# Kernel tuning notes

Measured on AMD Instinct MI355X. Metric: run time of the kernel, lower is better.

The kernel has to match this reference:

```python
import jax, jax.numpy as jnp
import numpy as np

N_HEAD, D_MODEL, D_K, D_V, POS_DIM = 8, 512, 64, 64, 2
TEMPERATURE = 8.0
LN_EPS = 1e-6


def setup_inputs() -> dict:
    key = jax.random.key(0)
    ks = jax.random.split(key, 16)
    B, S = 4, 1024
    s = 0.02
    return {
        "q": jax.random.normal(ks[0], (B, S, D_MODEL), jnp.float32),
        "k": jax.random.normal(ks[1], (B, S, D_MODEL), jnp.float32),
        "v": jax.random.normal(ks[2], (B, S, D_MODEL), jnp.float32),
        "pos_mat": jax.random.normal(ks[3], (S, S, POS_DIM), jnp.float32),
        "w_qs": jax.random.normal(ks[4], (N_HEAD * D_K, D_MODEL), jnp.float32) * s,
        "w_ks": jax.random.normal(ks[5], (N_HEAD * D_K, D_MODEL), jnp.float32) * s,
        "w_vs": jax.random.normal(ks[6], (N_HEAD * D_V, D_MODEL), jnp.float32) * s,
        "w_fc": jax.random.normal(ks[7], (D_MODEL, N_HEAD * D_V), jnp.float32) * s,
        "rp_w1": jax.random.normal(ks[8], (D_K, POS_DIM), jnp.float32) * s,
        "rp_b1": jnp.zeros((D_K,), jnp.float32),
        "rp_w2": jax.random.normal(ks[9], (D_K, D_K), jnp.float32) * s,
        "rp_b2": jnp.zeros((D_K,), jnp.float32),
        "ln_g": jnp.ones((D_MODEL,), jnp.float32),
        "ln_b": jnp.zeros((D_MODEL,), jnp.float32),
    }


def reference(q, k, v, pos_mat, w_qs, w_ks, w_vs, w_fc, rp_w1, rp_b1, rp_w2, rp_b2, ln_g, ln_b):
    B, S, _ = q.shape
    residual = q
    # projections -> (b, h, s, d)
    Q = (q @ w_qs.T).reshape(B, S, N_HEAD, D_K).transpose(0, 2, 1, 3)
    K = (k @ w_ks.T).reshape(B, S, N_HEAD, D_K).transpose(0, 2, 1, 3)
    V = (v @ w_vs.T).reshape(B, S, N_HEAD, D_V).transpose(0, 2, 1, 3)
    # relative position embedding: (s, s, d_k)
    a_k = jnp.tanh  # placeholder name avoided; compute MLP (no nonlinearity in original)
    a_k = (pos_mat @ rp_w1.T + rp_b1) @ rp_w2.T + rp_b2
    # sum over d_k of elementwise q*k*a_k, without materializing (b,h,q,k,d)
    attn = jnp.einsum("bhqd,bhkd,qkd->bhqk", Q, K, a_k) / TEMPERATURE
    attn = jax.nn.softmax(attn, axis=-1)  # dropout disabled (eval)
    out = jnp.einsum("bhqk,bhkd->bhqd", attn, V)  # (b,h,s,d_v)
    out = out.transpose(0, 2, 1, 3).reshape(B, S, N_HEAD * D_V)
    out = out @ w_fc.T + residual
    # layer norm
    mu = out.mean(-1, keepdims=True)
    var = out.var(-1, keepdims=True)
    out = (out - mu) / jnp.sqrt(var + LN_EPS) * ln_g + ln_b
    return (out, attn)
```

## Files before the change

kernel.cpp:

```cpp
#include <hip/hip_runtime.h>
#include <math.h>

#define NB   4
#define SEQ  1024
#define DMOD 512
#define NHD  8
#define DK   64

typedef unsigned short ushort_t;
typedef __attribute__((ext_vector_type(8))) short bf16x8;
typedef __attribute__((ext_vector_type(4))) float f32x4;

#define XQ_OFF   1024
#define XK_OFF   (XQ_OFF + 4194304)
#define XV_OFF   (XK_OFF + 4194304)
#define WQ_OFF   (XV_OFF + 4194304)
#define WK_OFF   (WQ_OFF + 524288)
#define WV_OFF   (WK_OFF + 524288)
#define WF_OFF   (WV_OFF + 524288)
#define QBF_OFF  (WF_OFF + 524288)
#define KBF_OFF  (QBF_OFF + 4194304)
#define VT_OFF   (KBF_OFF + 12582912)
#define POSBF_OFF XQ_OFF
#define O2_OFF   XQ_OFF
#define OBF_OFF  XV_OFF

__device__ inline ushort_t f2bf(float x) {
    unsigned u = __builtin_bit_cast(unsigned, x);
    unsigned r = (u + 0x7FFFu + ((u >> 16) & 1u)) >> 16;
    return (ushort_t)r;
}
__device__ inline unsigned pk2(float a, float b) {
    return (unsigned)f2bf(a) | ((unsigned)f2bf(b) << 16);
}

__global__ __launch_bounds__(256)
void setup_kernel(const float* __restrict__ pos,
                  const float* __restrict__ w_qs, const float* __restrict__ w_ks,
                  const float* __restrict__ w_vs, const float* __restrict__ w_fc,
                  const float* __restrict__ rp_w1, const float* __restrict__ rp_b1,
                  const float* __restrict__ rp_w2, const float* __restrict__ rp_b2,
                  unsigned* __restrict__ posbf,
                  ushort_t* __restrict__ WQ, ushort_t* __restrict__ WK,
                  ushort_t* __restrict__ WV, ushort_t* __restrict__ WF,
                  float* __restrict__ ws)
{
    const int bid = blockIdx.x;
    const int tid = threadIdx.x;
    if (bid < 1024) {
        int t = bid * 256 + tid;
        float4 a = *(const float4*)&pos[t * 8];
        float4 b = *(const float4*)&pos[t * 8 + 4];
        uint4 o = {pk2(a.x, a.y), pk2(a.z, a.w), pk2(b.x, b.y), pk2(b.z, b.w)};
        *(uint4*)&posbf[t * 4] = o;
    } else if (bid < 2048) {
        int which = (bid - 1024) >> 8;
        int t = ((bid - 1024) & 255) * 256 + tid;
        const float* s = (which == 0) ? w_qs : (which == 1) ? w_ks
                       : (which == 2) ? w_vs : w_fc;
        ushort_t* d = (which == 0) ? WQ : (which == 1) ? WK
                    : (which == 2) ? WV : WF;
        float4 v = *(const float4*)&s[t * 4];
        uint2 o = {pk2(v.x, v.y), pk2(v.z, v.w)};
        *(uint2*)&d[t * 4] = o;
    } else {
        __shared__ float red[4][64][3];
        int d = tid & 63, p = tid >> 6;
        float w0 = 0.f, w1 = 0.f, cc = 0.f;
        #pragma unroll
        for (int jj = 0; jj < 16; jj++) {
            int j = p * 16 + jj;
            float r2 = rp_w2[d * 64 + j];
            w0 += r2 * rp_w1[j * 2 + 0];
            w1 += r2 * rp_w1[j * 2 + 1];
            cc += r2 * rp_b1[j];
        }
        red[p][d][0] = w0; red[p][d][1] = w1; red[p][d][2] = cc;
        __syncthreads();
        if (p == 0) {
            w0 = red[0][d][0] + red[1][d][0] + red[2][d][0] + red[3][d][0];
            w1 = red[0][d][1] + red[1][d][1] + red[2][d][1] + red[3][d][1];
            cc = red[0][d][2] + red[1][d][2] + red[2][d][2] + red[3][d][2];
            ws[d] = cc + rp_b2[d];
            ws[64 + 2 * d + 0] = w0;
            ws[64 + 2 * d + 1] = w1;
        }
    }
}

#define GP 72

__global__ __launch_bounds__(256)
void mfma_gemm_qkv(const float* __restrict__ xq, const float* __restrict__ xk,
                   const float* __restrict__ xv,
                   const ushort_t* __restrict__ wq, const ushort_t* __restrict__ wk,
                   const ushort_t* __restrict__ wv,
                   ushort_t* __restrict__ Qbf, ushort_t* __restrict__ Kbf,
                   ushort_t* __restrict__ Vt, const float* __restrict__ wc)
{
    __shared__ ushort_t Sb[12800];
    ushort_t* Xs = Sb;
    ushort_t* Ws = Sb + 64 * GP;
    const int bz = blockIdx.z;
    const float* X = (bz == 0) ? xq : (bz == 1) ? xk : xv;
    const ushort_t* Wt = (bz == 0) ? wq : (bz == 1) ? wk : wv;
    const int n0 = blockIdx.y * 64;
    const int o0 = blockIdx.x * 64;
    const int tid = threadIdx.x;
    const int wave = tid >> 6, lane = tid & 63;
    const int m16 = lane & 15, g = lane >> 4;

    f32x4 acc[4] = {};
    for (int m0 = 0; m0 < 512; m0 += 64) {
        #pragma unroll
        for (int it = 0; it < 2; it++) {
            int idx = tid + it * 256;
            int row = idx >> 3, c8 = (idx & 7) * 8;
            float4 a = *(const float4*)&X[(n0 + row) * 512 + m0 + c8];
            float4 b = *(const float4*)&X[(n0 + row) * 512 + m0 + c8 + 4];
            uint4 o = {pk2(a.x, a.y), pk2(a.z, a.w), pk2(b.x, b.y), pk2(b.z, b.w)};
            *(uint4*)&Xs[row * GP + c8] = o;
            *(uint4*)&Ws[row * GP + c8] = *(const uint4*)&Wt[(o0 + row) * 512 + m0 + c8];
        }
        __syncthreads();
        #pragma unroll
        for (int kc = 0; kc < 2; kc++) {
            bf16x8 a = *(const bf16x8*)&Xs[(wave * 16 + m16) * GP + kc * 32 + g * 8];
            #pragma unroll
            for (int to = 0; to < 4; to++) {
                bf16x8 b = *(const bf16x8*)&Ws[(to * 16 + m16) * GP + kc * 32 + g * 8];
                acc[to] = __builtin_amdgcn_mfma_f32_16x16x32_bf16(a, b, acc[to], 0, 0, 0);
            }
        }
        __syncthreads();
    }

    const int b = n0 >> 10, s0 = n0 & 1023, h = o0 >> 6;
    const int bh = b * NHD + h;
    const int srow = wave * 16 + g * 4;

    if (bz == 0) {
        #pragma unroll
        for (int to = 0; to < 4; to++)
            #pragma unroll
            for (int r = 0; r < 4; r++)
                Sb[(srow + r) * GP + to * 16 + m16] = f2bf(acc[to][r]);
        __syncthreads();
        #pragma unroll
        for (int it = 0; it < 2; it++) {
            int cid = tid + it * 256;
            int row = cid >> 3, c8 = (cid & 7) * 8;
            *(uint4*)&Qbf[((bh << 10) + s0 + row) * 64 + c8] =
                *(const uint4*)&Sb[row * GP + c8];
        }
    } else if (bz == 1) {
        #pragma unroll
        for (int to = 0; to < 4; to++) {
            int d = to * 16 + m16;
            float c0 = wc[d], c1 = wc[64 + 2 * d], c2 = wc[64 + 2 * d + 1];
            #pragma unroll
            for (int r = 0; r < 4; r++) {
                float a = acc[to][r];
                int rb = (srow + r) * 200 + d;
                Sb[rb]       = f2bf(a * c0);
                Sb[rb + 64]  = f2bf(a * c1);
                Sb[rb + 128] = f2bf(a * c2);
            }
        }
        __syncthreads();
        #pragma unroll
        for (int it = 0; it < 6; it++) {
            int cid = tid + it * 256;
            int row = cid / 24, c = cid % 24;
            *(uint4*)&Kbf[((bh << 10) + s0 + row) * 192 + c * 8] =
                *(const uint4*)&Sb[row * 200 + c * 8];
        }
    } else {
        #pragma unroll
        for (int to = 0; to < 4; to++)
            #pragma unroll
            for (int r = 0; r < 4; r++)
                Sb[(to * 16 + m16) * GP + srow + r] = f2bf(acc[to][r]);
        __syncthreads();
        #pragma unroll
        for (int it = 0; it < 2; it++) {
            int cid = tid + it * 256;
            int row = cid >> 3, c8 = (cid & 7) * 8;
            *(uint4*)&Vt[(bh * 64 + row) * 1024 + s0 + c8] =
                *(const uint4*)&Sb[row * GP + c8];
        }
    }
}

__global__ __launch_bounds__(256)
void mfma_gemm_fc(const ushort_t* __restrict__ X, const ushort_t* __restrict__ Wt,
                  float* __restrict__ ofp, const float* __restrict__ resid)
{
    __shared__ ushort_t Xs[64 * GP];
    __shared__ ushort_t Ws[64 * GP];
    const int n0 = blockIdx.y * 64;
    const int o0 = blockIdx.x * 64;
    const int tid = threadIdx.x;
    const int wave = tid >> 6, lane = tid & 63;
    const int m16 = lane & 15, g = lane >> 4;

    f32x4 acc[4] = {};
    for (int m0 = 0; m0 < 512; m0 += 64) {
        #pragma unroll
        for (int it = 0; it < 2; it++) {
            int idx = tid + it * 256;
            int row = idx >> 3, c8 = (idx & 7) * 8;
            *(uint4*)&Xs[row * GP + c8] = *(const uint4*)&X[(n0 + row) * 512 + m0 + c8];
            *(uint4*)&Ws[row * GP + c8] = *(const uint4*)&Wt[(o0 + row) * 512 + m0 + c8];
        }
        __syncthreads();
        #pragma unroll
        for (int kc = 0; kc < 2; kc++) {
            bf16x8 a = *(const bf16x8*)&Xs[(wave * 16 + m16) * GP + kc * 32 + g * 8];
            #pragma unroll
            for (int to = 0; to < 4; to++) {
                bf16x8 b = *(const bf16x8*)&Ws[(to * 16 + m16) * GP + kc * 32 + g * 8];
                acc[to] = __builtin_amdgcn_mfma_f32_16x16x32_bf16(a, b, acc[to], 0, 0, 0);
            }
        }
        __syncthreads();
    }
    #pragma unroll
    for (int to = 0; to < 4; to++) {
        int o = o0 + to * 16 + m16;
        #pragma unroll
        for (int r = 0; r < 4; r++) {
            int n = n0 + wave * 16 + g * 4 + r;
            ofp[n * 512 + o] = acc[to][r] + resid[n * 512 + o];
        }
    }
}

#define QPITCH 72
#define KPLANE (64 * QPITCH + 8)
#define POSP 68
__global__ __launch_bounds__(256)
void fused_attn(const ushort_t* __restrict__ Qbf, const ushort_t* __restrict__ Kbf,
                const unsigned* __restrict__ posu, const ushort_t* __restrict__ Vt,
                float* __restrict__ attn, ushort_t* __restrict__ Obf)
{
    __shared__ ushort_t Ks[3 * KPLANE];
    __shared__ ushort_t Vs[64 * QPITCH];
    __shared__ ushort_t Ps[64 * QPITCH];
    __shared__ unsigned PosS[64 * POSP];
    const int bh = blockIdx.x;
    const int q0 = blockIdx.y * 64;
    const int tid = threadIdx.x;
    const int wave = tid >> 6, lane = tid & 63;
    const int m16 = lane & 15, g = lane >> 4;

    const ushort_t* qrow = &Qbf[((bh << 10) + q0 + wave * 16 + m16) * 64];
    bf16x8 qf0 = *(const bf16x8*)&qrow[g * 8];
    bf16x8 qf1 = *(const bf16x8*)&qrow[32 + g * 8];

    float l[4] = {0.f, 0.f, 0.f, 0.f};

    for (int k0 = 0; k0 < 1024; k0 += 64) {
        #pragma unroll
        for (int it = 0; it < 6; it++) {
            int idx = tid + it * 256;
            int row = idx / 24, c = idx % 24;
            int j = c >> 3, d8 = (c & 7) * 8;
            *(uint4*)&Ks[j * KPLANE + row * QPITCH + d8] =
                *(const uint4*)&Kbf[((bh << 10) + k0 + row) * 192 + c * 8];
        }
        #pragma unroll
        for (int it = 0; it < 4; it++) {
            int idx = tid + it * 256;
            int row = idx >> 4, c4 = (idx & 15) * 4;
            *(uint4*)&PosS[row * POSP + c4] =
                *(const uint4*)&posu[(q0 + row) * 1024 + k0 + c4];
        }
        __syncthreads();

        f32x4 sc[4][3] = {};
        #pragma unroll
        for (int kc = 0; kc < 2; kc++) {
            bf16x8 af = kc ? qf1 : qf0;
            #pragma unroll
            for (int tk = 0; tk < 4; tk++)
                #pragma unroll
                for (int j = 0; j < 3; j++) {
                    bf16x8 bfv = *(const bf16x8*)&Ks[j * KPLANE + (tk * 16 + m16) * QPITCH + kc * 32 + g * 8];
                    sc[tk][j] = __builtin_amdgcn_mfma_f32_16x16x32_bf16(af, bfv, sc[tk][j], 0, 0, 0);
                }
        }

        #pragma unroll
        for (int r = 0; r < 4; r++) {
            #pragma unroll
            for (int tk = 0; tk < 4; tk++) {
                unsigned pu = PosS[(wave * 16 + g * 4 + r) * POSP + tk * 16 + m16];
                float p0 = __builtin_bit_cast(float, pu << 16);
                float p1 = __builtin_bit_cast(float, pu & 0xFFFF0000u);
                float s = (sc[tk][0][r] + p0 * sc[tk][1][r] + p1 * sc[tk][2][r]) * 0.125f;
                l[r] += __expf(s);
            }
        }
        __syncthreads();
    }
    float inv_l[4];
    #pragma unroll
    for (int r = 0; r < 4; r++) {
        float s = l[r];
        #pragma unroll
        for (int msk = 1; msk < 16; msk <<= 1) s += __shfl_xor(s, msk, 64);
        inv_l[r] = 1.0f / s;
    }

    f32x4 ao[4] = {};
    for (int k0 = 0; k0 < 1024; k0 += 64) {
        #pragma unroll
        for (int it = 0; it < 6; it++) {
            int idx = tid + it * 256;
            int row = idx / 24, c = idx % 24;
            int j = c >> 3, d8 = (c & 7) * 8;
            *(uint4*)&Ks[j * KPLANE + row * QPITCH + d8] =
                *(const uint4*)&Kbf[((bh << 10) + k0 + row) * 192 + c * 8];
        }
        #pragma unroll
        for (int it = 0; it < 2; it++) {
            int idx = tid + it * 256;
            int row = idx >> 3, c8 = (idx & 7) * 8;
            *(uint4*)&Vs[row * QPITCH + c8] = *(const uint4*)&Vt[(bh * 64 + row) * 1024 + k0 + c8];
        }
        #pragma unroll
        for (int it = 0; it < 4; it++) {
            int idx = tid + it * 256;
            int row = idx >> 4, c4 = (idx & 15) * 4;
            *(uint4*)&PosS[row * POSP + c4] =
                *(const uint4*)&posu[(q0 + row) * 1024 + k0 + c4];
        }
        __syncthreads();

        f32x4 sc[4][3] = {};
        #pragma unroll
        for (int kc = 0; kc < 2; kc++) {
            bf16x8 af = kc ? qf1 : qf0;
            #pragma unroll
            for (int tk = 0; tk < 4; tk++)
                #pragma unroll
                for (int j = 0; j < 3; j++) {
                    bf16x8 bfv = *(const bf16x8*)&Ks[j * KPLANE + (tk * 16 + m16) * QPITCH + kc * 32 + g * 8];
                    sc[tk][j] = __builtin_amdgcn_mfma_f32_16x16x32_bf16(af, bfv, sc[tk][j], 0, 0, 0);
                }
        }

        #pragma unroll
        for (int r = 0; r < 4; r++) {
            int q = q0 + wave * 16 + g * 4 + r;
            #pragma unroll
            for (int tk = 0; tk < 4; tk++) {
                unsigned pu = PosS[(wave * 16 + g * 4 + r) * POSP + tk * 16 + m16];
                float p0 = __builtin_bit_cast(float, pu << 16);
                float p1 = __builtin_bit_cast(float, pu & 0xFFFF0000u);
                float s = (sc[tk][0][r] + p0 * sc[tk][1][r] + p1 * sc[tk][2][r]) * 0.125f;
                float p = __expf(s) * inv_l[r];
                attn[((bh << 10) + q) * 1024 + k0 + tk * 16 + m16] = p;
                Ps[(wave * 16 + g * 4 + r) * QPITCH + tk * 16 + m16] = f2bf(p);
            }
        }
        __syncthreads();

        #pragma unroll
        for (int kc = 0; kc < 2; kc++) {
            bf16x8 a = *(const bf16x8*)&Ps[(wave * 16 + m16) * QPITCH + kc * 32 + g * 8];
            #pragma unroll
            for (int td = 0; td < 4; td++) {
                bf16x8 b = *(const bf16x8*)&Vs[(td * 16 + m16) * QPITCH + kc * 32 + g * 8];
                ao[td] = __builtin_amdgcn_mfma_f32_16x16x32_bf16(a, b, ao[td], 0, 0, 0);
            }
        }
        __syncthreads();
    }

    const int b = bh >> 3, h = bh & 7;
    #pragma unroll
    for (int td = 0; td < 4; td++) {
        int d = td * 16 + m16;
        #pragma unroll
        for (int r = 0; r < 4; r++) {
            int q = q0 + wave * 16 + g * 4 + r;
            Obf[((b << 10) + q) * 512 + h * 64 + d] = f2bf(ao[td][r]);
        }
    }
}

__global__ __launch_bounds__(256)
void ln_kernel(const float* __restrict__ X, const float* __restrict__ g,
               const float* __restrict__ bta, float* __restrict__ out)
{
    const int row = blockIdx.x;
    const int tid = threadIdx.x;
    float2 x = *(const float2*)&X[row * 512 + tid * 2];
    float s  = x.x + x.y;
    float s2 = x.x * x.x + x.y * x.y;
    for (int off = 32; off; off >>= 1) {
        s  += __shfl_down(s, off, 64);
        s2 += __shfl_down(s2, off, 64);
    }
    __shared__ float rs[4], rs2[4];
    __shared__ float mu_s, rstd_s;
    int wave = tid >> 6, lane = tid & 63;
    if (lane == 0) { rs[wave] = s; rs2[wave] = s2; }
    __syncthreads();
    if (tid == 0) {
        float S1 = rs[0] + rs[1] + rs[2] + rs[3];
        float S2 = rs2[0] + rs2[1] + rs2[2] + rs2[3];
        float mu = S1 * (1.0f / 512.0f);
        float var = S2 * (1.0f / 512.0f) - mu * mu;
        mu_s = mu;
        rstd_s = rsqrtf(var + 1e-6f);
    }
    __syncthreads();
    float mu = mu_s, rstd = rstd_s;
    float2 gv = *(const float2*)&g[tid * 2];
    float2 bv = *(const float2*)&bta[tid * 2];
    float2 o;
    o.x = (x.x - mu) * rstd * gv.x + bv.x;
    o.y = (x.y - mu) * rstd * gv.y + bv.y;
    *(float2*)&out[row * 512 + tid * 2] = o;
}

extern "C" void kernel_launch(void* const* d_in, const int* in_sizes, int n_in,
                              void* d_out, int out_size, void* d_ws, size_t ws_size,
                              hipStream_t stream)
{
    const float* q       = (const float*)d_in[0];
    const float* k       = (const float*)d_in[1];
    const float* v       = (const float*)d_in[2];
    const float* pos_mat = (const float*)d_in[3];
    const float* w_qs    = (const float*)d_in[4];
    const float* w_ks    = (const float*)d_in[5];
    const float* w_vs    = (const float*)d_in[6];
    const float* w_fc    = (const float*)d_in[7];
    const float* rp_w1   = (const float*)d_in[8];
    const float* rp_b1   = (const float*)d_in[9];
    const float* rp_w2   = (const float*)d_in[10];
    const float* rp_b2   = (const float*)d_in[11];
    const float* ln_g    = (const float*)d_in[12];
    const float* ln_b    = (const float*)d_in[13];

    char* wsb = (char*)d_ws;
    float*    wc  = (float*)d_ws;
    ushort_t* WQ  = (ushort_t*)(wsb + WQ_OFF);
    ushort_t* WK  = (ushort_t*)(wsb + WK_OFF);
    ushort_t* WV  = (ushort_t*)(wsb + WV_OFF);
    ushort_t* WF  = (ushort_t*)(wsb + WF_OFF);
    ushort_t* Qbf = (ushort_t*)(wsb + QBF_OFF);
    ushort_t* Kbf = (ushort_t*)(wsb + KBF_OFF);
    ushort_t* Vt  = (ushort_t*)(wsb + VT_OFF);
    float*    O2  = (float*)(wsb + O2_OFF);
    ushort_t* Obf = (ushort_t*)(wsb + OBF_OFF);
    unsigned* Pbf = (unsigned*)(wsb + POSBF_OFF);

    float* out  = (float*)d_out;
    float* attn = out + 2097152;

    setup_kernel<<<dim3(2049), 256, 0, stream>>>(pos_mat, w_qs, w_ks, w_vs, w_fc,
                                                 rp_w1, rp_b1, rp_w2, rp_b2,
                                                 Pbf, WQ, WK, WV, WF, wc);

    mfma_gemm_qkv<<<dim3(8, 64, 3), 256, 0, stream>>>(q, k, v, WQ, WK, WV,
                                                      Qbf, Kbf, Vt, wc);

    fused_attn<<<dim3(32, 16), 256, 0, stream>>>(Qbf, Kbf, Pbf, Vt, attn, Obf);

    mfma_gemm_fc<<<dim3(8, 64), 256, 0, stream>>>(Obf, WF, O2, q);
    ln_kernel<<<dim3(4096), 256, 0, stream>>>(O2, ln_g, ln_b, out);
}
```

Before: 305.4 us.

## Double-buffer LDS tiles in QKV and FC GEMMs with register prefetch

Both projection GEMMs now prefetch the next K-slice from global memory into registers while the MFMAs consume the current tile. The staged data is then written to a second LDS buffer, which leaves one barrier per iteration instead of two. The grid axes are also swapped so consecutive blocks walk along rows rather than output columns, which changes L2 reuse of the activation and weight tiles. The cost is a larger LDS footprint (36KB) and more live registers, which may reduce occupancy.

```diff
diff --git a/kernel.cpp b/kernel.cpp
--- a/kernel.cpp
+++ b/kernel.cpp
@@ -98,31 +98,46 @@
                    ushort_t* __restrict__ Qbf, ushort_t* __restrict__ Kbf,
                    ushort_t* __restrict__ Vt, const float* __restrict__ wc)
 {
-    __shared__ ushort_t Sb[12800];
-    ushort_t* Xs = Sb;
-    ushort_t* Ws = Sb + 64 * GP;
+    __shared__ ushort_t SH[18432];
     const int bz = blockIdx.z;
     const float* X = (bz == 0) ? xq : (bz == 1) ? xk : xv;
     const ushort_t* Wt = (bz == 0) ? wq : (bz == 1) ? wk : wv;
-    const int n0 = blockIdx.y * 64;
-    const int o0 = blockIdx.x * 64;
+    const int n0 = blockIdx.x * 64;
+    const int o0 = blockIdx.y * 64;
     const int tid = threadIdx.x;
     const int wave = tid >> 6, lane = tid & 63;
     const int m16 = lane & 15, g = lane >> 4;
+    const int sr = tid >> 3, sc8 = (tid & 7) * 8;
+
+    float4 xa0, xb0, xa1, xb1;
+    uint4  wr0, wr1;
+
+#define LOADT(m0_) { \
+    xa0 = *(const float4*)&X[(n0 + sr) * 512 + (m0_) + sc8]; \
+    xb0 = *(const float4*)&X[(n0 + sr) * 512 + (m0_) + sc8 + 4]; \
+    xa1 = *(const float4*)&X[(n0 + sr + 32) * 512 + (m0_) + sc8]; \
+    xb1 = *(const float4*)&X[(n0 + sr + 32) * 512 + (m0_) + sc8 + 4]; \
+    wr0 = *(const uint4*)&Wt[(o0 + sr) * 512 + (m0_) + sc8]; \
+    wr1 = *(const uint4*)&Wt[(o0 + sr + 32) * 512 + (m0_) + sc8]; }
+#define STORET(b_) { \
+    ushort_t* Xs_ = SH + (b_) * 4608; \
+    ushort_t* Ws_ = SH + 9216 + (b_) * 4608; \
+    uint4 ox0 = {pk2(xa0.x, xa0.y), pk2(xa0.z, xa0.w), pk2(xb0.x, xb0.y), pk2(xb0.z, xb0.w)}; \
+    uint4 ox1 = {pk2(xa1.x, xa1.y), pk2(xa1.z, xa1.w), pk2(xb1.x, xb1.y), pk2(xb1.z, xb1.w)}; \
+    *(uint4*)&Xs_[sr * GP + sc8] = ox0; \
+    *(uint4*)&Xs_[(sr + 32) * GP + sc8] = ox1; \
+    *(uint4*)&Ws_[sr * GP + sc8] = wr0; \
+    *(uint4*)&Ws_[(sr + 32) * GP + sc8] = wr1; }
 
     f32x4 acc[4] = {};
+    LOADT(0); STORET(0);
+    __syncthreads();
+    int cur = 0;
     for (int m0 = 0; m0 < 512; m0 += 64) {
-        #pragma unroll
-        for (int it = 0; it < 2; it++) {
-            int idx = tid + it * 256;
-            int row = idx >> 3, c8 = (idx & 7) * 8;
-            float4 a = *(const float4*)&X[(n0 + row) * 512 + m0 + c8];
-            float4 b = *(const float4*)&X[(n0 + row) * 512 + m0 + c8 + 4];
-            uint4 o = {pk2(a.x, a.y), pk2(a.z, a.w), pk2(b.x, b.y), pk2(b.z, b.w)};
-            *(uint4*)&Xs[row * GP + c8] = o;
-            *(uint4*)&Ws[row * GP + c8] = *(const uint4*)&Wt[(o0 + row) * 512 + m0 + c8];
-        }
-        __syncthreads();
+        const int nxt = m0 + 64;
+        if (nxt < 512) LOADT(nxt);
+        const ushort_t* Xs = SH + cur * 4608;
+        const ushort_t* Ws = SH + 9216 + cur * 4608;
         #pragma unroll
         for (int kc = 0; kc < 2; kc++) {
             bf16x8 a = *(const bf16x8*)&Xs[(wave * 16 + m16) * GP + kc * 32 + g * 8];
@@ -132,8 +147,12 @@
                 acc[to] = __builtin_amdgcn_mfma_f32_16x16x32_bf16(a, b, acc[to], 0, 0, 0);
             }
         }
-        __syncthreads();
-    }
+        if (nxt < 512) STORET(cur ^ 1);
+        __syncthreads();
+        cur ^= 1;
+    }
+#undef LOADT
+#undef STORET
 
     const int b = n0 >> 10, s0 = n0 & 1023, h = o0 >> 6;
     const int bh = b * NHD + h;
@@ -144,14 +163,14 @@
         for (int to = 0; to < 4; to++)
             #pragma unroll
             for (int r = 0; r < 4; r++)
-                Sb[(srow + r) * GP + to * 16 + m16] = f2bf(acc[to][r]);
+                SH[(srow + r) * GP + to * 16 + m16] = f2bf(acc[to][r]);
         __syncthreads();
         #pragma unroll
         for (int it = 0; it < 2; it++) {
             int cid = tid + it * 256;
             int row = cid >> 3, c8 = (cid & 7) * 8;
             *(uint4*)&Qbf[((bh << 10) + s0 + row) * 64 + c8] =
-                *(const uint4*)&Sb[row * GP + c8];
+                *(const uint4*)&SH[row * GP + c8];
         }
     } else if (bz == 1) {
         #pragma unroll
@@ -162,9 +181,9 @@
             for (int r = 0; r < 4; r++) {
                 float a = acc[to][r];
                 int rb = (srow + r) * 200 + d;
-                Sb[rb]       = f2bf(a * c0);
-                Sb[rb + 64]  = f2bf(a * c1);
-                Sb[rb + 128] = f2bf(a * c2);
+                SH[rb]       = f2bf(a * c0);
+                SH[rb + 64]  = f2bf(a * c1);
+                SH[rb + 128] = f2bf(a * c2);
             }
         }
         __syncthreads();
@@ -173,21 +192,21 @@
             int cid = tid + it * 256;
             int row = cid / 24, c = cid % 24;
             *(uint4*)&Kbf[((bh << 10) + s0 + row) * 192 + c * 8] =
-                *(const uint4*)&Sb[row * 200 + c * 8];
+                *(const uint4*)&SH[row * 200 + c * 8];
         }
     } else {
         #pragma unroll
         for (int to = 0; to < 4; to++)
             #pragma unroll
             for (int r = 0; r < 4; r++)
-                Sb[(to * 16 + m16) * GP + srow + r] = f2bf(acc[to][r]);
+                SH[(to * 16 + m16) * GP + srow + r] = f2bf(acc[to][r]);
         __syncthreads();
         #pragma unroll
         for (int it = 0; it < 2; it++) {
             int cid = tid + it * 256;
             int row = cid >> 3, c8 = (cid & 7) * 8;
             *(uint4*)&Vt[(bh * 64 + row) * 1024 + s0 + c8] =
-                *(const uint4*)&Sb[row * GP + c8];
+                *(const uint4*)&SH[row * GP + c8];
         }
     }
 }
@@ -196,24 +215,38 @@
 void mfma_gemm_fc(const ushort_t* __restrict__ X, const ushort_t* __restrict__ Wt,
                   float* __restrict__ ofp, const float* __restrict__ resid)
 {
-    __shared__ ushort_t Xs[64 * GP];
-    __shared__ ushort_t Ws[64 * GP];
-    const int n0 = blockIdx.y * 64;
-    const int o0 = blockIdx.x * 64;
+    __shared__ ushort_t SH[18432];
+    const int n0 = blockIdx.x * 64;
+    const int o0 = blockIdx.y * 64;
     const int tid = threadIdx.x;
     const int wave = tid >> 6, lane = tid & 63;
     const int m16 = lane & 15, g = lane >> 4;
+    const int sr = tid >> 3, sc8 = (tid & 7) * 8;
+
+    uint4 xr0, xr1, wr0, wr1;
+
+#define LOADF(m0_) { \
+    xr0 = *(const uint4*)&X[(n0 + sr) * 512 + (m0_) + sc8]; \
+    xr1 = *(const uint4*)&X[(n0 + sr + 32) * 512 + (m0_) + sc8]; \
+    wr0 = *(const uint4*)&Wt[(o0 + sr) * 512 + (m0_) + sc8]; \
+    wr1 = *(const uint4*)&Wt[(o0 + sr + 32) * 512 + (m0_) + sc8]; }
+#define STOREF(b_) { \
+    ushort_t* Xs_ = SH + (b_) * 4608; \
+    ushort_t* Ws_ = SH + 9216 + (b_) * 4608; \
+    *(uint4*)&Xs_[sr * GP + sc8] = xr0; \
+    *(uint4*)&Xs_[(sr + 32) * GP + sc8] = xr1; \
+    *(uint4*)&Ws_[sr * GP + sc8] = wr0; \
+    *(uint4*)&Ws_[(sr + 32) * GP + sc8] = wr1; }
 
     f32x4 acc[4] = {};
+    LOADF(0); STOREF(0);
+    __syncthreads();
+    int cur = 0;
     for (int m0 = 0; m0 < 512; m0 += 64) {
-        #pragma unroll
-        for (int it = 0; it < 2; it++) {
-            int idx = tid + it * 256;
-            int row = idx >> 3, c8 = (idx & 7) * 8;
-            *(uint4*)&Xs[row * GP + c8] = *(const uint4*)&X[(n0 + row) * 512 + m0 + c8];
-            *(uint4*)&Ws[row * GP + c8] = *(const uint4*)&Wt[(o0 + row) * 512 + m0 + c8];
-        }
-        __syncthreads();
+        const int nxt = m0 + 64;
+        if (nxt < 512) LOADF(nxt);
+        const ushort_t* Xs = SH + cur * 4608;
+        const ushort_t* Ws = SH + 9216 + cur * 4608;
         #pragma unroll
         for (int kc = 0; kc < 2; kc++) {
             bf16x8 a = *(const bf16x8*)&Xs[(wave * 16 + m16) * GP + kc * 32 + g * 8];
@@ -223,8 +256,13 @@
                 acc[to] = __builtin_amdgcn_mfma_f32_16x16x32_bf16(a, b, acc[to], 0, 0, 0);
             }
         }
-        __syncthreads();
-    }
+        if (nxt < 512) STOREF(cur ^ 1);
+        __syncthreads();
+        cur ^= 1;
+    }
+#undef LOADF
+#undef STOREF
+
     #pragma unroll
     for (int to = 0; to < 4; to++) {
         int o = o0 + to * 16 + m16;
@@ -466,11 +504,11 @@
                                                  rp_w1, rp_b1, rp_w2, rp_b2,
                                                  Pbf, WQ, WK, WV, WF, wc);
 
-    mfma_gemm_qkv<<<dim3(8, 64, 3), 256, 0, stream>>>(q, k, v, WQ, WK, WV,
+    mfma_gemm_qkv<<<dim3(64, 8, 3), 256, 0, stream>>>(q, k, v, WQ, WK, WV,
                                                       Qbf, Kbf, Vt, wc);
 
     fused_attn<<<dim3(32, 16), 256, 0, stream>>>(Qbf, Kbf, Pbf, Vt, attn, Obf);
 
-    mfma_gemm_fc<<<dim3(8, 64), 256, 0, stream>>>(Obf, WF, O2, q);
+    mfma_gemm_fc<<<dim3(64, 8), 256, 0, stream>>>(Obf, WF, O2, q);
     ln_kernel<<<dim3(4096), 256, 0, stream>>>(O2, ln_g, ln_b, out);
 }
```

After: 281.6 us. 1.08x faster.

## Use 128x128 double-buffered register-prefetch tiles in QKV and FC GEMMs

Applied to the files above, without the earlier changes.

Both projection GEMMs move from 64x64 tiles with a single LDS buffer to 128x128 tiles. Each wave now computes a 64x64 subtile with a 4x4 MFMA grid, and the K-step is 32. Global loads for the next K-step are prefetched into registers and written to a second LDS buffer, so there is one barrier per step. The LDS-staged coalesced epilogue is replaced by direct scattered per-element bf16 stores, which may hurt write coalescing, especially for the transposed V output. Grid sizes shrink to 384 and 128 blocks, which could underfill the GPU's compute units.

```diff
diff --git a/kernel.cpp b/kernel.cpp
--- a/kernel.cpp
+++ b/kernel.cpp
@@ -88,8 +88,7 @@
     }
 }
 
-#define GP 72
-
+#define AP 40
 __global__ __launch_bounds__(256)
 void mfma_gemm_qkv(const float* __restrict__ xq, const float* __restrict__ xk,
                    const float* __restrict__ xv,
@@ -98,96 +97,91 @@
                    ushort_t* __restrict__ Qbf, ushort_t* __restrict__ Kbf,
                    ushort_t* __restrict__ Vt, const float* __restrict__ wc)
 {
-    __shared__ ushort_t Sb[12800];
-    ushort_t* Xs = Sb;
-    ushort_t* Ws = Sb + 64 * GP;
+    __shared__ ushort_t As[2][128 * AP];
+    __shared__ ushort_t Bs[2][128 * AP];
     const int bz = blockIdx.z;
     const float* X = (bz == 0) ? xq : (bz == 1) ? xk : xv;
     const ushort_t* Wt = (bz == 0) ? wq : (bz == 1) ? wk : wv;
-    const int n0 = blockIdx.y * 64;
-    const int o0 = blockIdx.x * 64;
+    const int n0 = blockIdx.x * 128;
+    const int o0 = blockIdx.y * 128;
     const int tid = threadIdx.x;
     const int wave = tid >> 6, lane = tid & 63;
     const int m16 = lane & 15, g = lane >> 4;
-
-    f32x4 acc[4] = {};
-    for (int m0 = 0; m0 < 512; m0 += 64) {
-        #pragma unroll
-        for (int it = 0; it < 2; it++) {
-            int idx = tid + it * 256;
-            int row = idx >> 3, c8 = (idx & 7) * 8;
-            float4 a = *(const float4*)&X[(n0 + row) * 512 + m0 + c8];
-            float4 b = *(const float4*)&X[(n0 + row) * 512 + m0 + c8 + 4];
-            uint4 o = {pk2(a.x, a.y), pk2(a.z, a.w), pk2(b.x, b.y), pk2(b.z, b.w)};
-            *(uint4*)&Xs[row * GP + c8] = o;
-            *(uint4*)&Ws[row * GP + c8] = *(const uint4*)&Wt[(o0 + row) * 512 + m0 + c8];
-        }
-        __syncthreads();
-        #pragma unroll
-        for (int kc = 0; kc < 2; kc++) {
-            bf16x8 a = *(const bf16x8*)&Xs[(wave * 16 + m16) * GP + kc * 32 + g * 8];
-            #pragma unroll
-            for (int to = 0; to < 4; to++) {
-                bf16x8 b = *(const bf16x8*)&Ws[(to * 16 + m16) * GP + kc * 32 + g * 8];
-                acc[to] = __builtin_amdgcn_mfma_f32_16x16x32_bf16(a, b, acc[to], 0, 0, 0);
+    const int wr = wave >> 1, wcol = wave & 1;
+
+    float4 ax[4];
+    uint4  bx[2];
+
+#define LOADA(k0_) { _Pragma("unroll") \
+    for (int it = 0; it < 4; it++) { \
+        int idx = tid + it * 256; \
+        int row = idx >> 3, c4 = (idx & 7) * 4; \
+        ax[it] = *(const float4*)&X[(n0 + row) * 512 + (k0_) + c4]; } }
+#define LOADB(k0_) { _Pragma("unroll") \
+    for (int it = 0; it < 2; it++) { \
+        int idx = tid + it * 256; \
+        int row = idx >> 2, c8 = (idx & 3) * 8; \
+        bx[it] = *(const uint4*)&Wt[(o0 + row) * 512 + (k0_) + c8]; } }
+#define STORES(b_) { _Pragma("unroll") \
+    for (int it = 0; it < 4; it++) { \
+        int idx = tid + it * 256; \
+        int row = idx >> 3, c4 = (idx & 7) * 4; \
+        uint2 o = {pk2(ax[it].x, ax[it].y), pk2(ax[it].z, ax[it].w)}; \
+        *(uint2*)&As[b_][row * AP + c4] = o; } \
+    _Pragma("unroll") \
+    for (int it = 0; it < 2; it++) { \
+        int idx = tid + it * 256; \
+        int row = idx >> 2, c8 = (idx & 3) * 8; \
+        *(uint4*)&Bs[b_][row * AP + c8] = bx[it]; } }
+
+    f32x4 acc[4][4] = {};
+    LOADA(0); LOADB(0); STORES(0);
+    __syncthreads();
+    int cur = 0;
+    for (int k0 = 0; k0 < 512; k0 += 32) {
+        if (k0 + 32 < 512) { LOADA(k0 + 32); LOADB(k0 + 32); }
+        bf16x8 af[4], bfr[4];
+        #pragma unroll
+        for (int m = 0; m < 4; m++)
+            af[m] = *(const bf16x8*)&As[cur][(wr * 64 + m * 16 + m16) * AP + g * 8];
+        #pragma unroll
+        for (int t = 0; t < 4; t++)
+            bfr[t] = *(const bf16x8*)&Bs[cur][(wcol * 64 + t * 16 + m16) * AP + g * 8];
+        #pragma unroll
+        for (int m = 0; m < 4; m++)
+            #pragma unroll
+            for (int t = 0; t < 4; t++)
+                acc[m][t] = __builtin_amdgcn_mfma_f32_16x16x32_bf16(af[m], bfr[t], acc[m][t], 0, 0, 0);
+        if (k0 + 32 < 512) STORES(cur ^ 1);
+        __syncthreads();
+        cur ^= 1;
+    }
+#undef LOADA
+#undef LOADB
+#undef STORES
+
+    #pragma unroll
+    for (int m = 0; m < 4; m++) {
+        #pragma unroll
+        for (int t = 0; t < 4; t++) {
+            int o = o0 + wcol * 64 + t * 16 + m16;
+            int h = o >> 6, d = o & 63;
+            #pragma unroll
+            for (int r = 0; r < 4; r++) {
+                int n = n0 + wr * 64 + m * 16 + g * 4 + r;
+                int b = n >> 10, s = n & 1023;
+                float a = acc[m][t][r];
+                if (bz == 0) {
+                    Qbf[(((b * NHD + h) << 10) + s) * 64 + d] = f2bf(a);
+                } else if (bz == 1) {
+                    int base = ((((b * NHD + h) << 10) + s) * 192) + d;
+                    Kbf[base]       = f2bf(a * wc[d]);
+                    Kbf[base + 64]  = f2bf(a * wc[64 + 2 * d + 0]);
+                    Kbf[base + 128] = f2bf(a * wc[64 + 2 * d + 1]);
+                } else {
+                    Vt[((b * NHD + h) * 64 + d) * 1024 + s] = f2bf(a);
+                }
             }
-        }
-        __syncthreads();
-    }
-
-    const int b = n0 >> 10, s0 = n0 & 1023, h = o0 >> 6;
-    const int bh = b * NHD + h;
-    const int srow = wave * 16 + g * 4;
-
-    if (bz == 0) {
-        #pragma unroll
-        for (int to = 0; to < 4; to++)
-            #pragma unroll
-            for (int r = 0; r < 4; r++)
-                Sb[(srow + r) * GP + to * 16 + m16] = f2bf(acc[to][r]);
-        __syncthreads();
-        #pragma unroll
-        for (int it = 0; it < 2; it++) {
-            int cid = tid + it * 256;
-            int row = cid >> 3, c8 = (cid & 7) * 8;
-            *(uint4*)&Qbf[((bh << 10) + s0 + row) * 64 + c8] =
-                *(const uint4*)&Sb[row * GP + c8];
-        }
-    } else if (bz == 1) {
-        #pragma unroll
-        for (int to = 0; to < 4; to++) {
-            int d = to * 16 + m16;
-            float c0 = wc[d], c1 = wc[64 + 2 * d], c2 = wc[64 + 2 * d + 1];
-            #pragma unroll
-            for (int r = 0; r < 4; r++) {
-                float a = acc[to][r];
-                int rb = (srow + r) * 200 + d;
-                Sb[rb]       = f2bf(a * c0);
-                Sb[rb + 64]  = f2bf(a * c1);
-                Sb[rb + 128] = f2bf(a * c2);
-            }
-        }
-        __syncthreads();
-        #pragma unroll
-        for (int it = 0; it < 6; it++) {
-            int cid = tid + it * 256;
-            int row = cid / 24, c = cid % 24;
-            *(uint4*)&Kbf[((bh << 10) + s0 + row) * 192 + c * 8] =
-                *(const uint4*)&Sb[row * 200 + c * 8];
-        }
-    } else {
-        #pragma unroll
-        for (int to = 0; to < 4; to++)
-            #pragma unroll
-            for (int r = 0; r < 4; r++)
-                Sb[(to * 16 + m16) * GP + srow + r] = f2bf(acc[to][r]);
-        __syncthreads();
-        #pragma unroll
-        for (int it = 0; it < 2; it++) {
-            int cid = tid + it * 256;
-            int row = cid >> 3, c8 = (cid & 7) * 8;
-            *(uint4*)&Vt[(bh * 64 + row) * 1024 + s0 + c8] =
-                *(const uint4*)&Sb[row * GP + c8];
         }
     }
 }
@@ -196,42 +190,70 @@
 void mfma_gemm_fc(const ushort_t* __restrict__ X, const ushort_t* __restrict__ Wt,
                   float* __restrict__ ofp, const float* __restrict__ resid)
 {
-    __shared__ ushort_t Xs[64 * GP];
-    __shared__ ushort_t Ws[64 * GP];
-    const int n0 = blockIdx.y * 64;
-    const int o0 = blockIdx.x * 64;
+    __shared__ ushort_t As[2][128 * AP];
+    __shared__ ushort_t Bs[2][128 * AP];
+    const int n0 = blockIdx.x * 128;
+    const int o0 = blockIdx.y * 128;
     const int tid = threadIdx.x;
     const int wave = tid >> 6, lane = tid & 63;
     const int m16 = lane & 15, g = lane >> 4;
-
-    f32x4 acc[4] = {};
-    for (int m0 = 0; m0 < 512; m0 += 64) {
-        #pragma unroll
-        for (int it = 0; it < 2; it++) {
-            int idx = tid + it * 256;
-            int row = idx >> 3, c8 = (idx & 7) * 8;
-            *(uint4*)&Xs[row * GP + c8] = *(const uint4*)&X[(n0 + row) * 512 + m0 + c8];
-            *(uint4*)&Ws[row * GP + c8] = *(const uint4*)&Wt[(o0 + row) * 512 + m0 + c8];
-        }
-        __syncthreads();
-        #pragma unroll
-        for (int kc = 0; kc < 2; kc++) {
-            bf16x8 a = *(const bf16x8*)&Xs[(wave * 16 + m16) * GP + kc * 32 + g * 8];
-            #pragma unroll
-            for (int to = 0; to < 4; to++) {
-                bf16x8 b = *(const bf16x8*)&Ws[(to * 16 + m16) * GP + kc * 32 + g * 8];
-                acc[to] = __builtin_amdgcn_mfma_f32_16x16x32_bf16(a, b, acc[to], 0, 0, 0);
+    const int wr = wave >> 1, wcol = wave & 1;
+
+    uint4 axr[2], bx[2];
+
+#define LOADAF(k0_) { _Pragma("unroll") \
+    for (int it = 0; it < 2; it++) { \
+        int idx = tid + it * 256; \
+        int row = idx >> 2, c8 = (idx & 3) * 8; \
+        axr[it] = *(const uint4*)&X[(n0 + row) * 512 + (k0_) + c8]; } }
+#define LOADBF(k0_) { _Pragma("unroll") \
+    for (int it = 0; it < 2; it++) { \
+        int idx = tid + it * 256; \
+        int row = idx >> 2, c8 = (idx & 3) * 8; \
+        bx[it] = *(const uint4*)&Wt[(o0 + row) * 512 + (k0_) + c8]; } }
+#define STORESF(b_) { _Pragma("unroll") \
+    for (int it = 0; it < 2; it++) { \
+        int idx = tid + it * 256; \
+        int row = idx >> 2, c8 = (idx & 3) * 8; \
+        *(uint4*)&As[b_][row * AP + c8] = axr[it]; \
+        *(uint4*)&Bs[b_][row * AP + c8] = bx[it]; } }
+
+    f32x4 acc[4][4] = {};
+    LOADAF(0); LOADBF(0); STORESF(0);
+    __syncthreads();
+    int cur = 0;
+    for (int k0 = 0; k0 < 512; k0 += 32) {
+        if (k0 + 32 < 512) { LOADAF(k0 + 32); LOADBF(k0 + 32); }
+        bf16x8 af[4], bfr[4];
+        #pragma unroll
+        for (int m = 0; m < 4; m++)
+            af[m] = *(const bf16x8*)&As[cur][(wr * 64 + m * 16 + m16) * AP + g * 8];
+        #pragma unroll
+        for (int t = 0; t < 4; t++)
+            bfr[t] = *(const bf16x8*)&Bs[cur][(wcol * 64 + t * 16 + m16) * AP + g * 8];
+        #pragma unroll
+        for (int m = 0; m < 4; m++)
+            #pragma unroll
+            for (int t = 0; t < 4; t++)
+                acc[m][t] = __builtin_amdgcn_mfma_f32_16x16x32_bf16(af[m], bfr[t], acc[m][t], 0, 0, 0);
+        if (k0 + 32 < 512) STORESF(cur ^ 1);
+        __syncthreads();
+        cur ^= 1;
+    }
+#undef LOADAF
+#undef LOADBF
+#undef STORESF
+
+    #pragma unroll
+    for (int m = 0; m < 4; m++) {
+        #pragma unroll
+        for (int t = 0; t < 4; t++) {
+            int o = o0 + wcol * 64 + t * 16 + m16;
+            #pragma unroll
+            for (int r = 0; r < 4; r++) {
+                int n = n0 + wr * 64 + m * 16 + g * 4 + r;
+                ofp[n * 512 + o] = acc[m][t][r] + resid[n * 512 + o];
             }
-        }
-        __syncthreads();
-    }
-    #pragma unroll
-    for (int to = 0; to < 4; to++) {
-        int o = o0 + to * 16 + m16;
-        #pragma unroll
-        for (int r = 0; r < 4; r++) {
-            int n = n0 + wave * 16 + g * 4 + r;
-            ofp[n * 512 + o] = acc[to][r] + resid[n * 512 + o];
         }
     }
 }
@@ -466,11 +488,11 @@
                                                  rp_w1, rp_b1, rp_w2, rp_b2,
                                                  Pbf, WQ, WK, WV, WF, wc);
 
-    mfma_gemm_qkv<<<dim3(8, 64, 3), 256, 0, stream>>>(q, k, v, WQ, WK, WV,
+    mfma_gemm_qkv<<<dim3(32, 4, 3), 256, 0, stream>>>(q, k, v, WQ, WK, WV,
                                                       Qbf, Kbf, Vt, wc);
 
     fused_attn<<<dim3(32, 16), 256, 0, stream>>>(Qbf, Kbf, Pbf, Vt, attn, Obf);
 
-    mfma_gemm_fc<<<dim3(8, 64), 256, 0, stream>>>(Obf, WF, O2, q);
+    mfma_gemm_fc<<<dim3(32, 4), 256, 0, stream>>>(Obf, WF, O2, q);
     ln_kernel<<<dim3(4096), 256, 0, stream>>>(O2, ln_g, ln_b, out);
 }
```

Result: slower. 326.3 us (+6.9%).
